# Performance work log

Hardware: AMD Instinct MI355X
Metric: run time of the kernel (lower is better)

Reference implementation:

```python
import jax, jax.numpy as jnp
import numpy as np

N_NODES = 20000
N_EDGES = 150000
IN_C = 512
OUT_C = 512
K_INIT = 7  # weight has K_INIT+1 = 8 slices, all used by the forward loop


def setup_inputs() -> dict:
    key = jax.random.key(0)
    k1, k2, k3, k4 = jax.random.split(key, 4)
    x = jax.random.normal(k1, (N_NODES, IN_C), dtype=jnp.float32)
    edge_index = jax.random.randint(k2, (2, N_EDGES), 0, N_NODES, dtype=jnp.int32)
    # uniform init as in reset_parameters: bound = 1/sqrt(in_channels * (K+1))
    bound = 1.0 / np.sqrt(IN_C * (K_INIT + 1))
    weight = jax.random.uniform(k3, (K_INIT + 1, IN_C, OUT_C), dtype=jnp.float32,
                                minval=-bound, maxval=bound)
    bias = jax.random.uniform(k4, (OUT_C,), dtype=jnp.float32,
                              minval=-bound, maxval=bound)
    return {"x": x, "edge_index": edge_index, "weight": weight, "bias": bias}


def _spmm(row, col, lap, x, num_nodes):
    # out[i] = sum_{e: row[e]==i} lap[e] * x[col[e]]
    msgs = lap[:, None] * x[col]  # [E, C] gather + scale
    return jax.ops.segment_sum(msgs, row, num_segments=num_nodes)


def reference(x, edge_index, weight, bias):
    row, col = edge_index[0], edge_index[1]
    num_nodes = x.shape[0]
    Kw = weight.shape[0]
    # degree^{-1/2} normalization of implicit adjacency, edge_attr = ones
    deg = jax.ops.segment_sum(jnp.ones_like(row, dtype=x.dtype), row,
                              num_segments=num_nodes)
    dinv = jnp.where(deg > 0, jax.lax.rsqrt(jnp.maximum(deg, 1e-30)), 0.0)
    lap = -dinv[row] * dinv[col]  # [E]
    Tx_0 = x
    out = Tx_0 @ weight[0]
    Tx_1 = _spmm(row, col, lap, x, num_nodes)
    out = out + Tx_1 @ weight[1]
    for k in range(2, Kw):
        Tx_2 = 2.0 * _spmm(row, col, lap, Tx_1, num_nodes) - Tx_0
        out = out + Tx_2 @ weight[k]
        Tx_0, Tx_1 = Tx_1, Tx_2
    return out + bias
```

## Files before the change

### kernel.cpp

```cpp
#include <hip/hip_runtime.h>

#define NN 20000
#define NP 20096
#define NE 150000
#define CC 512
#define KW 8
#define KT 4096
#define SCB 20

typedef __attribute__((ext_vector_type(8))) short short8;
typedef __attribute__((ext_vector_type(4))) float f32x4;
typedef __attribute__((ext_vector_type(4))) unsigned short ushort4v;
typedef __attribute__((ext_vector_type(8))) unsigned short ushort8v;

__device__ inline unsigned short f2bf(float f) {
  unsigned u = __builtin_bit_cast(unsigned, f);
  u += 0x7fffu + ((u >> 16) & 1u);
  return (unsigned short)(u >> 16);
}

__device__ inline float bf2f(unsigned short u) {
  return __builtin_bit_cast(float, (unsigned)u << 16);
}

__device__ inline void gload_lds16(const void* g, void* l) {
  __builtin_amdgcn_global_load_lds(
      (const __attribute__((address_space(1))) unsigned int*)g,
      (__attribute__((address_space(3))) unsigned int*)l, 16, 0, 0);
}


__global__ __launch_bounds__(256) void k_zero(int* __restrict__ deg, int* __restrict__ cursor) {
  int i = blockIdx.x * blockDim.x + threadIdx.x;
  if (i < NN) { deg[i] = 0; cursor[i] = 0; }
}

__global__ __launch_bounds__(256) void k_count(const int* __restrict__ row, int* __restrict__ deg) {
  int e = blockIdx.x * blockDim.x + threadIdx.x;
  if (e < NE) atomicAdd(&deg[row[e]], 1);
}

__global__ __launch_bounds__(256) void k_dinv(const int* __restrict__ deg, float* __restrict__ dinv) {
  int i = blockIdx.x * blockDim.x + threadIdx.x;
  if (i < NN) {
    int d = deg[i];
    dinv[i] = (d > 0) ? rsqrtf((float)d) : 0.0f;
  }
}

__global__ __launch_bounds__(1024) void k_scanA(const int* __restrict__ deg,
    int* __restrict__ row_off, int* __restrict__ bsum) {
  __shared__ int sm[1024];
  const int b = blockIdx.x, tid = threadIdx.x;
  int i = b * 1024 + tid;
  int v = (i < NN) ? deg[i] : 0;
  sm[tid] = v;
  __syncthreads();
  #pragma unroll
  for (int off = 1; off < 1024; off <<= 1) {
    int t = (tid >= off) ? sm[tid - off] : 0;
    __syncthreads();
    if (tid >= off) sm[tid] += t;
    __syncthreads();
  }
  if (i < NN) row_off[i] = sm[tid] - v;
  if (tid == 1023) bsum[b] = sm[1023];
}

__global__ __launch_bounds__(64) void k_scanB(int* __restrict__ bsum) {
  if (threadIdx.x == 0) {
    int run = 0;
    for (int b = 0; b < SCB; ++b) { int t = bsum[b]; bsum[b] = run; run += t; }
  }
}

__global__ __launch_bounds__(1024) void k_scanC(int* __restrict__ row_off, const int* __restrict__ bsum) {
  int i = blockIdx.x * 1024 + threadIdx.x;
  if (i < NN) row_off[i] += bsum[blockIdx.x];
  if (i == NN - 1) row_off[NN] = NE;
}

__global__ __launch_bounds__(256) void k_fill(const int* __restrict__ row, const int* __restrict__ col,
    const int* __restrict__ row_off, int* __restrict__ cursor, const float* __restrict__ dinv,
    int* __restrict__ csr_col, float* __restrict__ csr_val) {
  int e = blockIdx.x * blockDim.x + threadIdx.x;
  if (e < NE) {
    int r = row[e], c = col[e];
    int pos = row_off[r] + atomicAdd(&cursor[r], 1);
    csr_col[pos] = c;
    csr_val[pos] = -dinv[r] * dinv[c];
  }
}


__global__ __launch_bounds__(256) void k_wcast(const float* __restrict__ W, unsigned short* __restrict__ Bt) {
  __shared__ float sm[64][68];
  const int t = blockIdx.x;
  const int s = t >> 6;
  const int rem = t & 63;
  const int kt0 = (rem >> 3) * 64;
  const int nt0 = (rem & 7) * 64;
  const float* w = W + ((size_t)s << 18);
  const int tid = threadIdx.x;
  #pragma unroll
  for (int i = 0; i < 4; ++i) {
    int f = tid + i * 256;
    int r = f >> 4;
    int c4 = f & 15;
    float4 v = *(const float4*)&w[(size_t)(kt0 + r) * CC + nt0 + c4 * 4];
    sm[r][c4 * 4 + 0] = v.x; sm[r][c4 * 4 + 1] = v.y;
    sm[r][c4 * 4 + 2] = v.z; sm[r][c4 * 4 + 3] = v.w;
  }
  __syncthreads();
  #pragma unroll
  for (int i = 0; i < 2; ++i) {
    int g = tid + i * 256;
    int nl = g >> 3;
    int k8 = (g & 7) * 8;
    ushort8v o;
    #pragma unroll
    for (int j = 0; j < 8; ++j) o[j] = f2bf(sm[k8 + j][nl]);
    *(ushort8v*)&Bt[(size_t)(nt0 + nl) * KT + s * CC + kt0 + k8] = o;
  }
}

__global__ __launch_bounds__(256) void k_xcast(const float* __restrict__ x, unsigned short* __restrict__ txall) {
  size_t t = (size_t)blockIdx.x * 256 + threadIdx.x;
  size_t idx = t * 8;
  if (idx >= (size_t)NN * CC) return;
  size_t r = idx >> 9;
  int c = (int)(idx & 511);
  const float4* p = (const float4*)&x[idx];
  float4 a = p[0], b = p[1];
  ushort8v v;
  v[0] = f2bf(a.x); v[1] = f2bf(a.y); v[2] = f2bf(a.z); v[3] = f2bf(a.w);
  v[4] = f2bf(b.x); v[5] = f2bf(b.y); v[6] = f2bf(b.z); v[7] = f2bf(b.w);
  *(ushort8v*)&txall[r * KT + c] = v;
}


__global__ __launch_bounds__(256) void k_spmm(const unsigned short* __restrict__ gsrc,
    const unsigned short* __restrict__ gprev, unsigned short* __restrict__ gdst,
    const int* __restrict__ row_off, const int* __restrict__ csr_col,
    const float* __restrict__ csr_val, float alpha, float beta)
{
  __shared__ float4 smx[128];
  const int i = blockIdx.x;
  const int tid = threadIdx.x;
  const int es = tid >> 7;
  const int c = (tid & 127) * 4;
  const int e0 = row_off[i];
  const int e1 = row_off[i + 1];
  float4 a0 = make_float4(0.f,0.f,0.f,0.f), a1 = a0, a2 = a0, a3 = a0;
  int e = e0 + es;
  for (; e + 6 < e1; e += 8) {
    int j0 = csr_col[e], j1 = csr_col[e+2], j2 = csr_col[e+4], j3 = csr_col[e+6];
    float v0 = csr_val[e], v1 = csr_val[e+2], v2 = csr_val[e+4], v3 = csr_val[e+6];
    const ushort4v x0 = *(const ushort4v*)&gsrc[(size_t)j0 * KT + c];
    const ushort4v x1 = *(const ushort4v*)&gsrc[(size_t)j1 * KT + c];
    const ushort4v x2 = *(const ushort4v*)&gsrc[(size_t)j2 * KT + c];
    const ushort4v x3 = *(const ushort4v*)&gsrc[(size_t)j3 * KT + c];
    a0.x += v0*bf2f(x0[0]); a0.y += v0*bf2f(x0[1]); a0.z += v0*bf2f(x0[2]); a0.w += v0*bf2f(x0[3]);
    a1.x += v1*bf2f(x1[0]); a1.y += v1*bf2f(x1[1]); a1.z += v1*bf2f(x1[2]); a1.w += v1*bf2f(x1[3]);
    a2.x += v2*bf2f(x2[0]); a2.y += v2*bf2f(x2[1]); a2.z += v2*bf2f(x2[2]); a2.w += v2*bf2f(x2[3]);
    a3.x += v3*bf2f(x3[0]); a3.y += v3*bf2f(x3[1]); a3.z += v3*bf2f(x3[2]); a3.w += v3*bf2f(x3[3]);
  }
  for (; e < e1; e += 2) {
    int j = csr_col[e];
    float v = csr_val[e];
    const ushort4v xv = *(const ushort4v*)&gsrc[(size_t)j * KT + c];
    a0.x += v*bf2f(xv[0]); a0.y += v*bf2f(xv[1]); a0.z += v*bf2f(xv[2]); a0.w += v*bf2f(xv[3]);
  }
  float4 s;
  s.x = (a0.x + a1.x) + (a2.x + a3.x);
  s.y = (a0.y + a1.y) + (a2.y + a3.y);
  s.z = (a0.z + a1.z) + (a2.z + a3.z);
  s.w = (a0.w + a1.w) + (a2.w + a3.w);
  if (es == 1) smx[tid & 127] = s;
  __syncthreads();
  if (es == 0) {
    const float4 o = smx[tid];
    s.x += o.x; s.y += o.y; s.z += o.z; s.w += o.w;
    float4 r;
    if (beta != 0.0f) {
      const ushort4v p = *(const ushort4v*)&gprev[(size_t)i * KT + c];
      r.x = alpha * s.x + beta * bf2f(p[0]);
      r.y = alpha * s.y + beta * bf2f(p[1]);
      r.z = alpha * s.z + beta * bf2f(p[2]);
      r.w = alpha * s.w + beta * bf2f(p[3]);
    } else {
      r.x = alpha * s.x; r.y = alpha * s.y; r.z = alpha * s.z; r.w = alpha * s.w;
    }
    ushort4v bv;
    bv[0] = f2bf(r.x); bv[1] = f2bf(r.y); bv[2] = f2bf(r.z); bv[3] = f2bf(r.w);
    *(ushort4v*)&gdst[(size_t)i * KT + c] = bv;
  }
}


__global__ __launch_bounds__(256) void k_gemm(const unsigned short* __restrict__ A,
    const unsigned short* __restrict__ Bt, float* __restrict__ C,
    const float* __restrict__ bias)
{
  __shared__ unsigned short smA[128 * 32];
  __shared__ unsigned short smB[128 * 32];
  const int tid  = threadIdx.x;
  const int lane = tid & 63;
  const int wave = tid >> 6;
  const int wr = wave >> 1, wc = wave & 1;

  const int nwg = (NP / 128) * 4;
  int bid = blockIdx.x;
  int q = nwg >> 3, rr = nwg & 7;
  int xcd = bid & 7, lid = bid >> 3;
  int wgid = (xcd < rr ? xcd * (q + 1) : rr * (q + 1) + (xcd - rr) * q) + lid;
  const int m0 = (wgid >> 2) * 128;
  const int n0 = (wgid & 3) * 128;

  const int srow = lane >> 2;
  const int skc  = (lane & 3) * 8;

  f32x4 acc[4][4] = {};

  for (int k0 = 0; k0 < KT; k0 += 32) {
    #pragma unroll
    for (int i = 0; i < 2; ++i) {
      int row = wave * 32 + i * 16;
      gload_lds16(&A[(size_t)(m0 + row + srow) * KT + k0 + skc], &smA[row * 32]);
      gload_lds16(&Bt[(size_t)(n0 + row + srow) * KT + k0 + skc], &smB[row * 32]);
    }
    __syncthreads();

    short8 af[4], bfv[4];
    #pragma unroll
    for (int f = 0; f < 4; ++f) {
      af[f]  = *(const short8*)&smA[(wr * 64 + f * 16 + (lane & 15)) * 32 + (lane >> 4) * 8];
      bfv[f] = *(const short8*)&smB[(wc * 64 + f * 16 + (lane & 15)) * 32 + (lane >> 4) * 8];
    }
    #pragma unroll
    for (int fm = 0; fm < 4; ++fm)
      #pragma unroll
      for (int fn = 0; fn < 4; ++fn)
        acc[fm][fn] = __builtin_amdgcn_mfma_f32_16x16x32_bf16(af[fm], bfv[fn], acc[fm][fn], 0, 0, 0);
    __syncthreads();
  }

  const int prow = (lane >> 4) * 4;
  const int pcol = lane & 15;
  #pragma unroll
  for (int fm = 0; fm < 4; ++fm) {
    #pragma unroll
    for (int fn = 0; fn < 4; ++fn) {
      int gcol = n0 + wc * 64 + fn * 16 + pcol;
      float bb = bias[gcol];
      #pragma unroll
      for (int j = 0; j < 4; ++j) {
        int grow = m0 + wr * 64 + fm * 16 + prow + j;
        if (grow < NN) C[(size_t)grow * CC + gcol] = acc[fm][fn][j] + bb;
      }
    }
  }
}


extern "C" void kernel_launch(void* const* d_in, const int* in_sizes, int n_in,
                              void* d_out, int out_size, void* d_ws, size_t ws_size,
                              hipStream_t stream) {
  const float* x      = (const float*)d_in[0];
  const int*   row    = (const int*)d_in[1];
  const int*   col    = row + NE;
  const float* weight = (const float*)d_in[2];
  const float* bias   = (const float*)d_in[3];
  float* out = (float*)d_out;

  unsigned short* TxAll = (unsigned short*)d_ws;
  unsigned short* Bt    = TxAll + (size_t)NP * KT;
  float* dinv    = (float*)(Bt + (size_t)CC * KT);
  float* csr_val = dinv + NN;
  int*   deg     = (int*)(csr_val + NE);
  int*   cursor  = deg + NN;
  int*   row_off = cursor + NN;
  int*   csr_col = row_off + NN + 1;
  int*   bsum    = csr_col + NE;

  k_zero<<<(NN + 255) / 256, 256, 0, stream>>>(deg, cursor);
  k_count<<<(NE + 255) / 256, 256, 0, stream>>>(row, deg);
  k_dinv<<<(NN + 255) / 256, 256, 0, stream>>>(deg, dinv);
  k_scanA<<<SCB, 1024, 0, stream>>>(deg, row_off, bsum);
  k_scanB<<<1, 64, 0, stream>>>(bsum);
  k_scanC<<<SCB, 1024, 0, stream>>>(row_off, bsum);
  k_fill<<<(NE + 255) / 256, 256, 0, stream>>>(row, col, row_off, cursor, dinv, csr_col, csr_val);

  k_wcast<<<512, 256, 0, stream>>>(weight, Bt);
  k_xcast<<<(NN * CC / 8 + 255) / 256, 256, 0, stream>>>(x, TxAll);

  k_spmm<<<NN, 256, 0, stream>>>(TxAll, TxAll, TxAll + CC, row_off, csr_col, csr_val, 1.0f, 0.0f);
  for (int k = 2; k < KW; ++k)
    k_spmm<<<NN, 256, 0, stream>>>(TxAll + (size_t)(k - 1) * CC, TxAll + (size_t)(k - 2) * CC,
                                   TxAll + (size_t)k * CC, row_off, csr_col, csr_val, 2.0f, -1.0f);

  k_gemm<<<(NP / 128) * 4, 256, 0, stream>>>(TxAll, Bt, out, bias);
}
```

Measured before the change: 384.5 us.

## Restructure SpMM to tile nodes and channels per block

The SpMM kernel no longer launches one block per node. It launches 1256 blocks, each covering a 64-channel slice for 128 nodes, with 16 threads per node walking all of that node's edges and no shared-memory reduction or barrier. This cuts launch and block overhead and drops the per-node syncthreads. The cost is that each gather is now a 128-byte segment instead of the full row, and a serial loop of 8 rows per thread adds latency.

```diff
diff --git a/kernel.cpp b/kernel.cpp
--- a/kernel.cpp
+++ b/kernel.cpp
@@ -144,56 +144,56 @@
     const int* __restrict__ row_off, const int* __restrict__ csr_col,
     const float* __restrict__ csr_val, float alpha, float beta)
 {
-  __shared__ float4 smx[128];
-  const int i = blockIdx.x;
+  const int ct = blockIdx.x & 7;
+  const int nt = blockIdx.x >> 3;
   const int tid = threadIdx.x;
-  const int es = tid >> 7;
-  const int c = (tid & 127) * 4;
-  const int e0 = row_off[i];
-  const int e1 = row_off[i + 1];
-  float4 a0 = make_float4(0.f,0.f,0.f,0.f), a1 = a0, a2 = a0, a3 = a0;
-  int e = e0 + es;
-  for (; e + 6 < e1; e += 8) {
-    int j0 = csr_col[e], j1 = csr_col[e+2], j2 = csr_col[e+4], j3 = csr_col[e+6];
-    float v0 = csr_val[e], v1 = csr_val[e+2], v2 = csr_val[e+4], v3 = csr_val[e+6];
-    const ushort4v x0 = *(const ushort4v*)&gsrc[(size_t)j0 * KT + c];
-    const ushort4v x1 = *(const ushort4v*)&gsrc[(size_t)j1 * KT + c];
-    const ushort4v x2 = *(const ushort4v*)&gsrc[(size_t)j2 * KT + c];
-    const ushort4v x3 = *(const ushort4v*)&gsrc[(size_t)j3 * KT + c];
-    a0.x += v0*bf2f(x0[0]); a0.y += v0*bf2f(x0[1]); a0.z += v0*bf2f(x0[2]); a0.w += v0*bf2f(x0[3]);
-    a1.x += v1*bf2f(x1[0]); a1.y += v1*bf2f(x1[1]); a1.z += v1*bf2f(x1[2]); a1.w += v1*bf2f(x1[3]);
-    a2.x += v2*bf2f(x2[0]); a2.y += v2*bf2f(x2[1]); a2.z += v2*bf2f(x2[2]); a2.w += v2*bf2f(x2[3]);
-    a3.x += v3*bf2f(x3[0]); a3.y += v3*bf2f(x3[1]); a3.z += v3*bf2f(x3[2]); a3.w += v3*bf2f(x3[3]);
-  }
-  for (; e < e1; e += 2) {
-    int j = csr_col[e];
-    float v = csr_val[e];
-    const ushort4v xv = *(const ushort4v*)&gsrc[(size_t)j * KT + c];
-    a0.x += v*bf2f(xv[0]); a0.y += v*bf2f(xv[1]); a0.z += v*bf2f(xv[2]); a0.w += v*bf2f(xv[3]);
-  }
-  float4 s;
-  s.x = (a0.x + a1.x) + (a2.x + a3.x);
-  s.y = (a0.y + a1.y) + (a2.y + a3.y);
-  s.z = (a0.z + a1.z) + (a2.z + a3.z);
-  s.w = (a0.w + a1.w) + (a2.w + a3.w);
-  if (es == 1) smx[tid & 127] = s;
-  __syncthreads();
-  if (es == 0) {
-    const float4 o = smx[tid];
-    s.x += o.x; s.y += o.y; s.z += o.z; s.w += o.w;
-    float4 r;
+  const int nl = tid >> 4;
+  const int cb = ct * 64 + (tid & 15) * 4;
+
+  #pragma unroll 1
+  for (int r = 0; r < 8; ++r) {
+    const int i = nt * 128 + r * 16 + nl;
+    if (i >= NN) continue;
+    const int e0 = row_off[i];
+    const int e1 = row_off[i + 1];
+    float4 a0 = make_float4(0.f,0.f,0.f,0.f), a1 = a0, a2 = a0, a3 = a0;
+    int e = e0;
+    for (; e + 3 < e1; e += 4) {
+      int j0 = csr_col[e], j1 = csr_col[e+1], j2 = csr_col[e+2], j3 = csr_col[e+3];
+      float v0 = csr_val[e], v1 = csr_val[e+1], v2 = csr_val[e+2], v3 = csr_val[e+3];
+      const ushort4v x0 = *(const ushort4v*)&gsrc[(size_t)j0 * KT + cb];
+      const ushort4v x1 = *(const ushort4v*)&gsrc[(size_t)j1 * KT + cb];
+      const ushort4v x2 = *(const ushort4v*)&gsrc[(size_t)j2 * KT + cb];
+      const ushort4v x3 = *(const ushort4v*)&gsrc[(size_t)j3 * KT + cb];
+      a0.x += v0*bf2f(x0[0]); a0.y += v0*bf2f(x0[1]); a0.z += v0*bf2f(x0[2]); a0.w += v0*bf2f(x0[3]);
+      a1.x += v1*bf2f(x1[0]); a1.y += v1*bf2f(x1[1]); a1.z += v1*bf2f(x1[2]); a1.w += v1*bf2f(x1[3]);
+      a2.x += v2*bf2f(x2[0]); a2.y += v2*bf2f(x2[1]); a2.z += v2*bf2f(x2[2]); a2.w += v2*bf2f(x2[3]);
+      a3.x += v3*bf2f(x3[0]); a3.y += v3*bf2f(x3[1]); a3.z += v3*bf2f(x3[2]); a3.w += v3*bf2f(x3[3]);
+    }
+    for (; e < e1; ++e) {
+      int j = csr_col[e];
+      float v = csr_val[e];
+      const ushort4v xv = *(const ushort4v*)&gsrc[(size_t)j * KT + cb];
+      a0.x += v*bf2f(xv[0]); a0.y += v*bf2f(xv[1]); a0.z += v*bf2f(xv[2]); a0.w += v*bf2f(xv[3]);
+    }
+    float4 s;
+    s.x = (a0.x + a1.x) + (a2.x + a3.x);
+    s.y = (a0.y + a1.y) + (a2.y + a3.y);
+    s.z = (a0.z + a1.z) + (a2.z + a3.z);
+    s.w = (a0.w + a1.w) + (a2.w + a3.w);
+    float4 rr;
     if (beta != 0.0f) {
-      const ushort4v p = *(const ushort4v*)&gprev[(size_t)i * KT + c];
-      r.x = alpha * s.x + beta * bf2f(p[0]);
-      r.y = alpha * s.y + beta * bf2f(p[1]);
-      r.z = alpha * s.z + beta * bf2f(p[2]);
-      r.w = alpha * s.w + beta * bf2f(p[3]);
+      const ushort4v p = *(const ushort4v*)&gprev[(size_t)i * KT + cb];
+      rr.x = alpha * s.x + beta * bf2f(p[0]);
+      rr.y = alpha * s.y + beta * bf2f(p[1]);
+      rr.z = alpha * s.z + beta * bf2f(p[2]);
+      rr.w = alpha * s.w + beta * bf2f(p[3]);
     } else {
-      r.x = alpha * s.x; r.y = alpha * s.y; r.z = alpha * s.z; r.w = alpha * s.w;
+      rr.x = alpha * s.x; rr.y = alpha * s.y; rr.z = alpha * s.z; rr.w = alpha * s.w;
     }
     ushort4v bv;
-    bv[0] = f2bf(r.x); bv[1] = f2bf(r.y); bv[2] = f2bf(r.z); bv[3] = f2bf(r.w);
-    *(ushort4v*)&gdst[(size_t)i * KT + c] = bv;
+    bv[0] = f2bf(rr.x); bv[1] = f2bf(rr.y); bv[2] = f2bf(rr.z); bv[3] = f2bf(rr.w);
+    *(ushort4v*)&gdst[(size_t)i * KT + cb] = bv;
   }
 }
 
@@ -294,10 +294,11 @@
   k_wcast<<<512, 256, 0, stream>>>(weight, Bt);
   k_xcast<<<(NN * CC / 8 + 255) / 256, 256, 0, stream>>>(x, TxAll);
 
-  k_spmm<<<NN, 256, 0, stream>>>(TxAll, TxAll, TxAll + CC, row_off, csr_col, csr_val, 1.0f, 0.0f);
+  const int spmm_grid = 157 * 8;
+  k_spmm<<<spmm_grid, 256, 0, stream>>>(TxAll, TxAll, TxAll + CC, row_off, csr_col, csr_val, 1.0f, 0.0f);
   for (int k = 2; k < KW; ++k)
-    k_spmm<<<NN, 256, 0, stream>>>(TxAll + (size_t)(k - 1) * CC, TxAll + (size_t)(k - 2) * CC,
-                                   TxAll + (size_t)k * CC, row_off, csr_col, csr_val, 2.0f, -1.0f);
+    k_spmm<<<spmm_grid, 256, 0, stream>>>(TxAll + (size_t)(k - 1) * CC, TxAll + (size_t)(k - 2) * CC,
+                                          TxAll + (size_t)k * CC, row_off, csr_col, csr_val, 2.0f, -1.0f);
 
   k_gemm<<<(NP / 128) * 4, 256, 0, stream>>>(TxAll, Bt, out, bias);
 }
```

After: 439.8 us. 1.14x slower.
